# Optimization experiments

Measured on AMD Instinct MI355X. Metric: run time of the kernel, lower is better.

## Reference

```python
import jax, jax.numpy as jnp
import numpy as np

D = 400   # d_model
H = 16    # num heads
KD = 400  # keras MHA key_dim (per-head dim)
GU = 1800 # GRU units
EPS = 1e-6


def _ln(x, g, b):
    m = jnp.mean(x, -1, keepdims=True)
    v = jnp.mean((x - m) ** 2, -1, keepdims=True)
    return (x - m) * jax.lax.rsqrt(v + EPS) * g + b


def _gru_step(x, K, RK, B):
    # Single timestep keras GRU (reset_after=True, activation=elu, h0=0).
    h0 = jnp.zeros((x.shape[0], RK.shape[0]), x.dtype)
    xz, xr, xh = jnp.split(x @ K + B[0], 3, axis=-1)
    rz, rr, rh = jnp.split(h0 @ RK + B[1], 3, axis=-1)
    z = jax.nn.sigmoid(xz + rz)
    r = jax.nn.sigmoid(xr + rr)
    hh = jax.nn.elu(xh + r * rh)
    return z * h0 + (1.0 - z) * hh


def _forward(x, Wq, bq, Wk, bk, Wv, bv, Wo, bo, ln1_g, ln1_b,
             ffn_w1, ffn_b1, ffn_w2, ffn_b2, ln2_g, ln2_b,
             gru_fk, gru_frk, gru_fb, gru_bk, gru_brk, gru_bb,
             d2_w, d2_b, d4_w, d4_b, out_w, out_b):
    # The original python loop over growing prefixes is equivalent to one
    # batched encoder pass over inputs[1:, -1:, :] (seq_len==1, so MHA is
    # per-batch-element independent), with the raw row inputs[0] prepended.
    xe = x[1:, -1:, :]  # [N-1, 1, D]
    q = jnp.einsum('bsd,dhk->bshk', xe, Wq) + bq
    k = jnp.einsum('bsd,dhk->bshk', xe, Wk) + bk
    v = jnp.einsum('bsd,dhk->bshk', xe, Wv) + bv
    logits = jnp.einsum('bqhk,bmhk->bhqm', q, k) / jnp.sqrt(jnp.float32(KD))
    probs = jax.nn.softmax(logits, axis=-1)  # trivially ones (seq=1)
    ctx = jnp.einsum('bhqm,bmhk->bqhk', probs, v)
    attn = jnp.einsum('bqhk,hkd->bqd', ctx, Wo) + bo
    out1 = _ln(xe + attn, ln1_g, ln1_b)
    ffn = jax.nn.relu(out1 @ ffn_w1 + ffn_b1) @ ffn_w2 + ffn_b2
    enc = _ln(out1 + ffn, ln2_g, ln2_b)  # [N-1, 1, D]
    output = jnp.concatenate([x[:1, -1:, :], enc], axis=0)  # [N, 1, D]
    upd = jnp.concatenate([x, output], axis=1)              # [N, 4, D]
    flat = upd.reshape(x.shape[0], -1)                      # [N, 1600]
    # frozen cite_cos_sim_model (inference: dropout layers are identity)
    hf = _gru_step(flat, gru_fk, gru_frk, gru_fb)
    hb = _gru_step(flat, gru_bk, gru_brk, gru_bb)
    x1 = jnp.concatenate([hf, hb], axis=-1)   # [N, 3600]
    x3 = jax.nn.elu(x1 @ d2_w + d2_b)         # [N, 1800]
    x5 = jax.nn.elu(x3 @ d4_w + d4_b)         # [N, 1800]
    cat = jnp.concatenate([x1, x3, x5], axis=-1)  # [N, 7200]
    return cat @ out_w + out_b                # [N, 140]


def setup_inputs() -> dict:
    key = jax.random.key(0)
    shapes = {
        'Wq': (D, H, KD), 'bq': (H, KD), 'Wk': (D, H, KD), 'bk': (H, KD),
        'Wv': (D, H, KD), 'bv': (H, KD), 'Wo': (H, KD, D), 'bo': (D,),
        'ln1_b': (D,), 'ffn_w1': (D, 2), 'ffn_b1': (2,), 'ffn_w2': (2, D),
        'ffn_b2': (D,), 'ln2_b': (D,),
        'gru_fk': (1600, 3 * GU), 'gru_frk': (GU, 3 * GU), 'gru_fb': (2, 3 * GU),
        'gru_bk': (1600, 3 * GU), 'gru_brk': (GU, 3 * GU), 'gru_bb': (2, 3 * GU),
        'd2_w': (2 * GU, GU), 'd2_b': (GU,), 'd4_w': (GU, GU), 'd4_b': (GU,),
        'out_w': (4 * GU, 140), 'out_b': (140,),
    }
    keys = jax.random.split(key, len(shapes) + 1)
    inp = {'x': jax.random.normal(keys[0], (16384, 3, D), jnp.float32)}
    for i, (name, sh) in enumerate(shapes.items()):
        inp[name] = jax.random.normal(keys[i + 1], sh, jnp.float32) * 0.02
    inp['ln1_g'] = jnp.ones((D,), jnp.float32)
    inp['ln2_g'] = jnp.ones((D,), jnp.float32)
    return inp


def reference(x, Wq, bq, Wk, bk, Wv, bv, Wo, bo, ln1_g, ln1_b,
              ffn_w1, ffn_b1, ffn_w2, ffn_b2, ln2_g, ln2_b,
              gru_fk, gru_frk, gru_fb, gru_bk, gru_brk, gru_bb,
              d2_w, d2_b, d4_w, d4_b, out_w, out_b):
    return _forward(x, Wq, bq, Wk, bk, Wv, bv, Wo, bo, ln1_g, ln1_b,
                    ffn_w1, ffn_b1, ffn_w2, ffn_b2, ln2_g, ln2_b,
                    gru_fk, gru_frk, gru_fb, gru_bk, gru_brk, gru_bb,
                    d2_w, d2_b, d4_w, d4_b, out_w, out_b)
```

## Files before the change

kernel.cpp:

```cpp
#include <hip/hip_runtime.h>
#include <hip/hip_bf16.h>

typedef unsigned short u16;
using bf16x8 = __attribute__((ext_vector_type(8))) short;
using f32x4  = __attribute__((ext_vector_type(4))) float;

#define CM 2048
#define NC 8

#define P_LN1G 0
#define P_LN1B 400
#define P_FW1  800
#define P_FB1  1600
#define P_FW2  1602
#define P_FB2  2402
#define P_LN2G 2802
#define P_LN2B 3202
#define P_GFB  3602
#define P_GBB  14402
#define P_BV   25202
#define P_BO   31602
#define P_OB   32002
#define P_END  32142

__device__ __forceinline__ u16 f2bf(float f) {
  unsigned u = __float_as_uint(f);
  unsigned r = u + 0x7FFFu + ((u >> 16) & 1u);
  return (u16)(r >> 16);
}
__device__ __forceinline__ float bf2f(u16 h) {
  return __uint_as_float(((unsigned)h) << 16);
}

__device__ __forceinline__ void gl_lds16(const u16* g, u16* l) {
  __builtin_amdgcn_global_load_lds(
      (__attribute__((address_space(1))) void*)g,
      (__attribute__((address_space(3))) void*)l, 16, 0, 0);
}

__global__ void detect_dtype(int* flag, const void* x) {
  if (threadIdx.x == 0 && blockIdx.x == 0) {
    const u16* p = (const u16*)x;
    int cnt = 0;
    for (int i = 0; i < 64; i++) {
      int e = (p[2 * i] >> 7) & 0xFF;
      if (e >= 0x70 && e <= 0x85) cnt++;
    }
    *flag = (cnt >= 32) ? 1 : 0;
  }
}

__global__ void canon_bf(u16* __restrict__ dst, const void* __restrict__ src,
                         int n, const int* __restrict__ flag) {
  int i = blockIdx.x * 256 + threadIdx.x;
  if (i >= n) return;
  dst[i] = (*flag) ? ((const u16*)src)[i] : f2bf(((const float*)src)[i]);
}

__global__ void canon_x_rows(u16* __restrict__ dst, const void* __restrict__ src,
                             long base, int n, const int* __restrict__ flag) {
  int i = blockIdx.x * 256 + threadIdx.x;
  if (i >= n) return;
  long j = base + i;
  dst[i] = (*flag) ? ((const u16*)src)[j] : f2bf(((const float*)src)[j]);
}

__global__ void canon_f32k(float* __restrict__ dst, const void* __restrict__ src,
                           int n, const int* __restrict__ flag) {
  int i = blockIdx.x * 256 + threadIdx.x;
  if (i >= n) return;
  dst[i] = (*flag) ? bf2f(((const u16*)src)[i]) : ((const float*)src)[i];
}

__global__ void f32_to_bf(u16* __restrict__ dst, const float* __restrict__ src, int n) {
  int i = blockIdx.x * 256 + threadIdx.x;
  if (i < n) dst[i] = f2bf(src[i]);
}

template <int EPI, bool CL>
__global__ __launch_bounds__(256) void gemm_bt(
    const u16* __restrict__ A, const u16* __restrict__ Bt, void* __restrict__ Cv,
    const float* __restrict__ bias, int M, int N, int K, int lda, int ldb, int ldc,
    const u16* aend)
{
  __shared__ u16 lsA[128 * 32];
  __shared__ u16 lsB[128 * 32];
  const int tid = threadIdx.x;
  const int m0 = blockIdx.x * 128, n0 = blockIdx.y * 128;
  const int wave = tid >> 6, lane = tid & 63;
  const int wm = (wave >> 1) << 6, wn = (wave & 1) << 6;
  const int quad = lane >> 4, l16 = lane & 15;

  int ra = m0 + (tid >> 2);       if (ra > M - 1) ra = M - 1;
  int ra2 = m0 + 64 + (tid >> 2); if (ra2 > M - 1) ra2 = M - 1;
  int rb = n0 + (tid >> 2);       if (rb > N - 1) rb = N - 1;
  int rb2 = n0 + 64 + (tid >> 2); if (rb2 > N - 1) rb2 = N - 1;
  const u16* Ag  = A + (size_t)ra * lda + (tid & 3) * 8;
  const u16* Ag2 = A + (size_t)ra2 * lda + (tid & 3) * 8;
  const u16* Bg  = Bt + (size_t)rb * ldb + (tid & 3) * 8;
  const u16* Bg2 = Bt + (size_t)rb2 * ldb + (tid & 3) * 8;
  u16* la = lsA + tid * 8;
  u16* lb = lsB + tid * 8;

  f32x4 acc[4][4];
#pragma unroll
  for (int i = 0; i < 4; i++)
#pragma unroll
    for (int j = 0; j < 4; j++) acc[i][j] = (f32x4){0.f, 0.f, 0.f, 0.f};

  for (int k0 = 0; k0 < K; k0 += 32) {
    __syncthreads();
    const u16* pa  = Ag + k0;
    const u16* pa2 = Ag2 + k0;
    if (CL) { if (pa > aend) pa = aend; if (pa2 > aend) pa2 = aend; }
    gl_lds16(pa, la);
    gl_lds16(pa2, la + 2048);
    gl_lds16(Bg + k0, lb);
    gl_lds16(Bg2 + k0, lb + 2048);
    __syncthreads();
    bf16x8 af[4], bfv[4];
#pragma unroll
    for (int t = 0; t < 4; t++) {
      af[t]  = *(const bf16x8*)(lsA + ((wm + t * 16 + l16) << 5) + (quad << 3));
      bfv[t] = *(const bf16x8*)(lsB + ((wn + t * 16 + l16) << 5) + (quad << 3));
    }
#pragma unroll
    for (int mt = 0; mt < 4; mt++)
#pragma unroll
      for (int nt = 0; nt < 4; nt++)
        acc[mt][nt] = __builtin_amdgcn_mfma_f32_16x16x32_bf16(af[mt], bfv[nt], acc[mt][nt], 0, 0, 0);
  }

#pragma unroll
  for (int mt = 0; mt < 4; mt++)
#pragma unroll
    for (int r = 0; r < 4; r++) {
      const int row = m0 + wm + mt * 16 + quad * 4 + r;
      if (row < M) {
#pragma unroll
        for (int nt = 0; nt < 4; nt++) {
          const int col = n0 + wn + nt * 16 + l16;
          if (col < N) {
            float v = acc[mt][nt][r];
            if (EPI == 0) ((u16*)Cv)[(size_t)row * ldc + col] = f2bf(v);
            if (EPI == 1) ((float*)Cv)[(size_t)row * ldc + col] = v + bias[col];
            if (EPI == 2) {
              float p = v + bias[col];
              ((u16*)Cv)[(size_t)row * ldc + col] = f2bf(p > 0.f ? p : expm1f(p));
            }
          }
        }
      }
    }
}

__global__ __launch_bounds__(256) void gemm_bt_sk(
    const u16* __restrict__ A, const u16* __restrict__ Bt, float* __restrict__ outf,
    int M, int N, int K, int lda, int ldb, int ldc)
{
  __shared__ u16 lsA[128 * 32];
  __shared__ u16 lsB[128 * 32];
  const int tid = threadIdx.x;
  const int m0 = blockIdx.x * 128, n0 = blockIdx.y * 128;
  const int wave = tid >> 6, lane = tid & 63;
  const int wm = (wave >> 1) << 6, wn = (wave & 1) << 6;
  const int quad = lane >> 4, l16 = lane & 15;
  const int S = K >> 5, kz = blockIdx.z, KS = gridDim.z;
  const int s0 = (S * kz) / KS, s1 = (S * (kz + 1)) / KS;

  int ra = m0 + (tid >> 2);       if (ra > M - 1) ra = M - 1;
  int ra2 = m0 + 64 + (tid >> 2); if (ra2 > M - 1) ra2 = M - 1;
  int rb = n0 + (tid >> 2);       if (rb > N - 1) rb = N - 1;
  int rb2 = n0 + 64 + (tid >> 2); if (rb2 > N - 1) rb2 = N - 1;
  const u16* Ag  = A + (size_t)ra * lda + (tid & 3) * 8;
  const u16* Ag2 = A + (size_t)ra2 * lda + (tid & 3) * 8;
  const u16* Bg  = Bt + (size_t)rb * ldb + (tid & 3) * 8;
  const u16* Bg2 = Bt + (size_t)rb2 * ldb + (tid & 3) * 8;
  u16* la = lsA + tid * 8;
  u16* lb = lsB + tid * 8;

  f32x4 acc[4][4];
#pragma unroll
  for (int i = 0; i < 4; i++)
#pragma unroll
    for (int j = 0; j < 4; j++) acc[i][j] = (f32x4){0.f, 0.f, 0.f, 0.f};

  for (int s = s0; s < s1; ++s) {
    const int k0 = s << 5;
    __syncthreads();
    gl_lds16(Ag + k0, la);
    gl_lds16(Ag2 + k0, la + 2048);
    gl_lds16(Bg + k0, lb);
    gl_lds16(Bg2 + k0, lb + 2048);
    __syncthreads();
    bf16x8 af[4], bfv[4];
#pragma unroll
    for (int t = 0; t < 4; t++) {
      af[t]  = *(const bf16x8*)(lsA + ((wm + t * 16 + l16) << 5) + (quad << 3));
      bfv[t] = *(const bf16x8*)(lsB + ((wn + t * 16 + l16) << 5) + (quad << 3));
    }
#pragma unroll
    for (int mt = 0; mt < 4; mt++)
#pragma unroll
      for (int nt = 0; nt < 4; nt++)
        acc[mt][nt] = __builtin_amdgcn_mfma_f32_16x16x32_bf16(af[mt], bfv[nt], acc[mt][nt], 0, 0, 0);
  }

#pragma unroll
  for (int mt = 0; mt < 4; mt++)
#pragma unroll
    for (int r = 0; r < 4; r++) {
      const int row = m0 + wm + mt * 16 + quad * 4 + r;
      if (row < M) {
#pragma unroll
        for (int nt = 0; nt < 4; nt++) {
          const int col = n0 + wn + nt * 16 + l16;
          if (col < N) atomicAdd(&outf[(size_t)row * ldc + col], acc[mt][nt][r]);
        }
      }
    }
}

__global__ __launch_bounds__(256) void transpose_bf(
    u16* __restrict__ dst, const void* __restrict__ src, int SR, int SC, int DR, int DC,
    const int* __restrict__ flag)
{
  __shared__ u16 t[32][33];
  const int fl = *flag;
  const int tx = threadIdx.x & 31, ty = threadIdx.x >> 5;
  const int j0 = blockIdx.x << 5;
  const int i0 = blockIdx.y << 5;
#pragma unroll
  for (int s = 0; s < 32; s += 8) {
    int sr = j0 + ty + s, sc = i0 + tx;
    u16 v = 0;
    if (sr < SR && sc < SC) {
      size_t idx = (size_t)sr * SC + sc;
      v = fl ? ((const u16*)src)[idx] : f2bf(((const float*)src)[idx]);
    }
    t[ty + s][tx] = v;
  }
  __syncthreads();
#pragma unroll
  for (int s = 0; s < 32; s += 8) {
    int dr = i0 + ty + s, dc = j0 + tx;
    if (dr < DR && dc < DC) dst[(size_t)dr * DC + dc] = t[tx][ty + s];
  }
}

__global__ void build_outT(u16* __restrict__ dst, const void* __restrict__ ow,
                           const int* __restrict__ flag) {
  const int fl = *flag;
  int idx = blockIdx.x * 256 + threadIdx.x;
  if (idx >= 140 * 7264) return;
  int o = idx / 7264, c = idx - o * 7264;
  long si = -1;
  if (c < 3600) si = (long)c * 140 + o;
  else if (c >= 3616 && c < 5416) si = (long)(c - 16) * 140 + o;
  else if (c >= 5440 && c < 7240) si = (long)(c - 40) * 140 + o;
  u16 v = 0;
  if (si >= 0) v = fl ? ((const u16*)ow)[si] : f2bf(((const float*)ow)[si]);
  dst[idx] = v;
}

__global__ void zero_u32(unsigned* p, int n) {
  int i = blockIdx.x * 256 + threadIdx.x;
  if (i < n) p[i] = 0;
}

__global__ void zero_catpads(u16* cat, int rows) {
  int idx = blockIdx.x * 256 + threadIdx.x;
  if (idx >= rows * 64) return;
  int b = idx >> 6, t = idx & 63;
  int col = t < 16 ? 3600 + t : (t < 40 ? 5400 + t : 7200 + t);
  cat[(size_t)b * 7264 + col] = 0;
}

__global__ void init_outf(float* __restrict__ outf, const u16* __restrict__ pbuf) {
  int i = blockIdx.x * 256 + threadIdx.x;
  if (i < 16384 * 140) outf[i] = bf2f(pbuf[P_OB + i % 140]);
}

__device__ __forceinline__ void block_sum2(float& a, float& b, float* red, int t) {
#pragma unroll
  for (int o = 32; o > 0; o >>= 1) { a += __shfl_down(a, o, 64); b += __shfl_down(b, o, 64); }
  __syncthreads();
  if ((t & 63) == 0) { red[t >> 6] = a; red[4 + (t >> 6)] = b; }
  __syncthreads();
  a = red[0] + red[1] + red[2] + red[3];
  b = red[4] + red[5] + red[6] + red[7];
}

__global__ __launch_bounds__(256) void c0_kernel(float* c0, const u16* __restrict__ WoT,
                                                 const u16* __restrict__ pbuf) {
  __shared__ float red[8];
  int d = blockIdx.x, t = threadIdx.x;
  const u16* row = WoT + (size_t)d * 6400;
  const u16* bv = pbuf + P_BV;
  float s = 0.f;
  for (int j = t; j < 6400; j += 256) s += bf2f(bv[j]) * bf2f(row[j]);
  float dummy = 0.f;
  block_sum2(s, dummy, red, t);
  if (t == 0) c0[d] = s + bf2f(pbuf[P_BO + d]);
}

__global__ __launch_bounds__(256) void enc_rows(
    const u16* __restrict__ xc, const float* __restrict__ attn,
    const u16* __restrict__ pbuf, u16* __restrict__ flatc, int r0)
{
  __shared__ float red[8];
  const int li = blockIdx.x, t = threadIdx.x;
  const int gr = r0 + li;
  const u16* xr = xc + (size_t)li * 1200;
  u16* fr = flatc + (size_t)li * 1600;
  if (t < 150) ((uint4*)fr)[t] = ((const uint4*)xr)[t];
  if (gr == 0) {
    if (t < 50) ((uint4*)(fr + 1200))[t] = ((const uint4*)(xr + 800))[t];
    return;
  }
  const u16* xe = xr + 800;
  const float* at = attn + (size_t)li * 400;
  const u16 *g1 = pbuf + P_LN1G, *b1 = pbuf + P_LN1B, *fw1 = pbuf + P_FW1,
            *fb1v = pbuf + P_FB1, *fw2 = pbuf + P_FW2, *fb2v = pbuf + P_FB2,
            *g2 = pbuf + P_LN2G, *b2 = pbuf + P_LN2B;
  const int i1 = t + 256;
  float a0 = bf2f(xe[t]) + at[t];
  float a1 = 0.f;
  if (i1 < 400) a1 = bf2f(xe[i1]) + at[i1];
  float s = a0 + a1, ss = a0 * a0 + a1 * a1;
  block_sum2(s, ss, red, t);
  float mean = s * (1.f / 400.f);
  float var = ss * (1.f / 400.f) - mean * mean;
  float rstd = rsqrtf(var + 1e-6f);
  float o0 = (a0 - mean) * rstd * bf2f(g1[t]) + bf2f(b1[t]);
  float o1 = 0.f;
  if (i1 < 400) o1 = (a1 - mean) * rstd * bf2f(g1[i1]) + bf2f(b1[i1]);
  float d0 = o0 * bf2f(fw1[2 * t]), d1 = o0 * bf2f(fw1[2 * t + 1]);
  if (i1 < 400) { d0 += o1 * bf2f(fw1[2 * i1]); d1 += o1 * bf2f(fw1[2 * i1 + 1]); }
  block_sum2(d0, d1, red, t);
  float t0 = d0 + bf2f(fb1v[0]); t0 = t0 > 0.f ? t0 : 0.f;
  float t1 = d1 + bf2f(fb1v[1]); t1 = t1 > 0.f ? t1 : 0.f;
  float c0v = o0 + t0 * bf2f(fw2[t]) + t1 * bf2f(fw2[400 + t]) + bf2f(fb2v[t]);
  float c1v = 0.f;
  if (i1 < 400) c1v = o1 + t0 * bf2f(fw2[i1]) + t1 * bf2f(fw2[400 + i1]) + bf2f(fb2v[i1]);
  s = c0v + c1v; ss = c0v * c0v + c1v * c1v;
  block_sum2(s, ss, red, t);
  mean = s * (1.f / 400.f);
  var = ss * (1.f / 400.f) - mean * mean;
  rstd = rsqrtf(var + 1e-6f);
  u16* dr = fr + 1200;
  dr[t] = f2bf((c0v - mean) * rstd * bf2f(g2[t]) + bf2f(b2[t]));
  if (i1 < 400) dr[i1] = f2bf((c1v - mean) * rstd * bf2f(g2[i1]) + bf2f(b2[i1]));
}

__global__ __launch_bounds__(256) void gru_act(
    const u16* __restrict__ G, int ldg, const u16* __restrict__ pbuf, int boff,
    u16* __restrict__ cat, int off, int rows)
{
  int idx = blockIdx.x * 256 + threadIdx.x;
  if (idx >= rows * 1800) return;
  int b = idx / 1800, u = idx - b * 1800;
  const u16* g = G + (size_t)b * ldg;
  const u16* B = pbuf + boff;
  float xz = bf2f(g[u]) + bf2f(B[u]) + bf2f(B[5400 + u]);
  float xr = bf2f(g[1800 + u]) + bf2f(B[1800 + u]) + bf2f(B[7200 + u]);
  float xh = bf2f(g[3600 + u]) + bf2f(B[3600 + u]);
  float rh = bf2f(B[9000 + u]);
  float z = 1.f / (1.f + expf(-xz));
  float r = 1.f / (1.f + expf(-xr));
  float pre = xh + r * rh;
  float hh = pre > 0.f ? pre : expm1f(pre);
  cat[(size_t)b * 7264 + off + u] = f2bf((1.f - z) * hh);
}

extern "C" void kernel_launch(void* const* d_in, const int* in_sizes, int n_in,
                              void* d_out, int out_size, void* d_ws, size_t ws_size,
                              hipStream_t stream) {
  static const int MAP_DICT[22] = {5,6,7,8, 9,10,11,12,13,14, 15,17,18,20, 21,22,23,24, 25,26, 27,28};
  static const int MAP_SIG[22]  = {5,6,7,8, 10,11,12,13,14,16, 17,19,20,22, 23,24,25,26, 27,28, 9,15};
  const int* MAP = (in_sizes[15] > 100000) ? MAP_DICT : MAP_SIG;

  const void* x    = d_in[0];
  const void* Wv   = d_in[MAP[0]];
  const void* bv   = d_in[MAP[1]];
  const void* Wo   = d_in[MAP[2]];
  const void* bo   = d_in[MAP[3]];
  const void* ln1b = d_in[MAP[4]];
  const void* fw1  = d_in[MAP[5]];
  const void* fb1  = d_in[MAP[6]];
  const void* fw2  = d_in[MAP[7]];
  const void* fb2  = d_in[MAP[8]];
  const void* ln2b = d_in[MAP[9]];
  const void* gfk  = d_in[MAP[10]];
  const void* gfb  = d_in[MAP[11]];
  const void* gbk  = d_in[MAP[12]];
  const void* gbb  = d_in[MAP[13]];
  const void* d2w  = d_in[MAP[14]];
  const void* d2b  = d_in[MAP[15]];
  const void* d4w  = d_in[MAP[16]];
  const void* d4b  = d_in[MAP[17]];
  const void* ow   = d_in[MAP[18]];
  const void* ob   = d_in[MAP[19]];
  const void* ln1g = d_in[MAP[20]];
  const void* ln2g = d_in[MAP[21]];
  float* outf = (float*)d_out;

  unsigned char* base = (unsigned char*)d_ws;
  size_t off = 0;
  auto take = [&](size_t bytes) -> void* {
    void* p = base + off;
    off += (bytes + 255) & ~(size_t)255;
    return p;
  };
  u16*   KfT   = (u16*)take((size_t)5400 * 1600 * 2);
  u16*   KbT   = (u16*)take((size_t)5400 * 1600 * 2);
  u16*   d2T   = (u16*)take((size_t)1800 * 3616 * 2);
  u16*   d4T   = (u16*)take((size_t)1800 * 1824 * 2);
  u16*   outT  = (u16*)take((size_t)140 * 7264 * 2);
  u16*   WoT   = (u16*)take((size_t)400 * 6400 * 2);
  u16*   MT    = (u16*)take((size_t)400 * 416 * 2);
  float* MTf   = (float*)take((size_t)400 * 416 * 4);
  u16*   pbuf  = (u16*)take((size_t)P_END * 2);
  int*   flag  = (int*)take(256);
  float* c0    = (float*)take(400 * 4);
  float* d2bf  = (float*)take(1800 * 4);
  float* d4bf  = (float*)take(1800 * 4);

  int CMV = 0;
  {
    const size_t avail  = ws_size > off ? ws_size - off : 0;
    const size_t perrow = (size_t)(1600 + 10800 + 7264) * 2;
    const size_t margin = (size_t)4 << 20;
    if      (avail >= (size_t)16384 * perrow + margin) CMV = 16384;
    else if (avail >= (size_t)8192  * perrow + margin) CMV = 8192;
    else if (avail >= (size_t)4096  * perrow + margin) CMV = 4096;
    else if (avail >= (size_t)2048  * perrow + margin) CMV = 2048;
  }

  u16 *flatc, *Gc, *catc;
  if (CMV) {
    flatc = (u16*)take((size_t)CMV * 1600 * 2);
    Gc    = (u16*)take((size_t)CMV * 10800 * 2);
    catc  = (u16*)take((size_t)CMV * 7264 * 2);
  } else {
    flatc = (u16*)take((size_t)CM * 1600 * 2);
    Gc    = (u16*)take((size_t)CM * 5400 * 2);
    catc  = (u16*)take((size_t)CM * 7264 * 2);
  }
  const int rows = CMV ? CMV : CM;
  float* attnc = (float*)Gc;
  u16*   xc    = (u16*)((unsigned char*)Gc + (size_t)rows * 1600);
  u16*   Wvc   = catc;

  detect_dtype<<<1, 64, 0, stream>>>(flag, x);
  canon_bf<<<2, 256, 0, stream>>>(pbuf + P_LN1G, ln1g, 400, flag);
  canon_bf<<<2, 256, 0, stream>>>(pbuf + P_LN1B, ln1b, 400, flag);
  canon_bf<<<4, 256, 0, stream>>>(pbuf + P_FW1, fw1, 800, flag);
  canon_bf<<<1, 256, 0, stream>>>(pbuf + P_FB1, fb1, 2, flag);
  canon_bf<<<4, 256, 0, stream>>>(pbuf + P_FW2, fw2, 800, flag);
  canon_bf<<<2, 256, 0, stream>>>(pbuf + P_FB2, fb2, 400, flag);
  canon_bf<<<2, 256, 0, stream>>>(pbuf + P_LN2G, ln2g, 400, flag);
  canon_bf<<<2, 256, 0, stream>>>(pbuf + P_LN2B, ln2b, 400, flag);
  canon_bf<<<43, 256, 0, stream>>>(pbuf + P_GFB, gfb, 10800, flag);
  canon_bf<<<43, 256, 0, stream>>>(pbuf + P_GBB, gbb, 10800, flag);
  canon_bf<<<25, 256, 0, stream>>>(pbuf + P_BV, bv, 6400, flag);
  canon_bf<<<2, 256, 0, stream>>>(pbuf + P_BO, bo, 400, flag);
  canon_bf<<<1, 256, 0, stream>>>(pbuf + P_OB, ob, 140, flag);
  canon_f32k<<<8, 256, 0, stream>>>(d2bf, d2b, 1800, flag);
  canon_f32k<<<8, 256, 0, stream>>>(d4bf, d4b, 1800, flag);

  transpose_bf<<<dim3(50, 169), 256, 0, stream>>>(KfT, gfk, 1600, 5400, 5400, 1600, flag);
  transpose_bf<<<dim3(50, 169), 256, 0, stream>>>(KbT, gbk, 1600, 5400, 5400, 1600, flag);
  transpose_bf<<<dim3(113, 57), 256, 0, stream>>>(d2T, d2w, 3600, 1800, 1800, 3616, flag);
  transpose_bf<<<dim3(57, 57), 256, 0, stream>>>(d4T, d4w, 1800, 1800, 1800, 1824, flag);
  transpose_bf<<<dim3(200, 13), 256, 0, stream>>>(WoT, Wo, 6400, 400, 400, 6400, flag);
  build_outT<<<(140 * 7264 + 255) / 256, 256, 0, stream>>>(outT, ow, flag);
  init_outf<<<(16384 * 140 + 255) / 256, 256, 0, stream>>>(outf, pbuf);
  c0_kernel<<<400, 256, 0, stream>>>(c0, WoT, pbuf);

  canon_bf<<<10000, 256, 0, stream>>>(Wvc, Wv, 2560000, flag);
  zero_u32<<<(166400 + 255) / 256, 256, 0, stream>>>((unsigned*)MTf, 166400);
  gemm_bt_sk<<<dim3(4, 4, 16), 256, 0, stream>>>(WoT, Wvc, MTf,
      400, 400, 6400, 6400, 6400, 416);
  f32_to_bf<<<(166400 + 255) / 256, 256, 0, stream>>>(MT, MTf, 166400);

  if (CMV) {
    zero_catpads<<<(CMV * 64 + 255) / 256, 256, 0, stream>>>(catc, CMV);
    const int nchunk = 16384 / CMV;
    for (int c = 0; c < nchunk; ++c) {
      const long r0 = (long)c * CMV;
      canon_x_rows<<<(CMV * 1200 + 255) / 256, 256, 0, stream>>>(
          xc, x, r0 * 1200, CMV * 1200, flag);
      gemm_bt<1, true><<<dim3(CMV / 128, 4), 256, 0, stream>>>(
          xc + 800, MT, attnc, c0, CMV, 400, 416, 1200, 416, 400,
          xc + (size_t)CMV * 1200 - 8);
      enc_rows<<<CMV, 256, 0, stream>>>(xc, attnc, pbuf, flatc, (int)r0);
      gemm_bt<0, false><<<dim3(CMV / 128, 85), 256, 0, stream>>>(
          flatc, KfT, Gc, nullptr, CMV, 10800, 1600, 1600, 1600, 10800, nullptr);
      gru_act<<<(CMV * 1800 + 255) / 256, 256, 0, stream>>>(
          Gc, 10800, pbuf, P_GFB, catc, 0, CMV);
      gru_act<<<(CMV * 1800 + 255) / 256, 256, 0, stream>>>(
          Gc + 5400, 10800, pbuf, P_GBB, catc, 1800, CMV);
      gemm_bt<2, false><<<dim3(CMV / 128, 15), 256, 0, stream>>>(
          catc, d2T, catc + 3616, d2bf, CMV, 1800, 3616, 7264, 3616, 7264, nullptr);
      gemm_bt<2, false><<<dim3(CMV / 128, 15), 256, 0, stream>>>(
          catc + 3616, d4T, catc + 5440, d4bf, CMV, 1800, 1824, 7264, 1824, 7264, nullptr);
      gemm_bt_sk<<<dim3(CMV / 128, 2, 8), 256, 0, stream>>>(
          catc, outT, outf + (size_t)r0 * 140, CMV, 140, 7264, 7264, 7264, 140);
    }
  } else {
    zero_catpads<<<(CM * 64 + 255) / 256, 256, 0, stream>>>(catc, CM);
    for (int c = 0; c < NC; ++c) {
      const int r0 = c * CM;
      canon_x_rows<<<(CM * 1200 + 255) / 256, 256, 0, stream>>>(
          xc, x, (long)r0 * 1200, CM * 1200, flag);
      gemm_bt<1, true><<<dim3(CM / 128, 4), 256, 0, stream>>>(
          xc + 800, MT, attnc, c0, CM, 400, 416, 1200, 416, 400,
          xc + (size_t)CM * 1200 - 8);
      enc_rows<<<CM, 256, 0, stream>>>(xc, attnc, pbuf, flatc, r0);
      gemm_bt<0, false><<<dim3(CM / 128, 43), 256, 0, stream>>>(
          flatc, KfT, Gc, nullptr, CM, 5400, 1600, 1600, 1600, 5400, nullptr);
      gru_act<<<(CM * 1800 + 255) / 256, 256, 0, stream>>>(
          Gc, 5400, pbuf, P_GFB, catc, 0, CM);
      gemm_bt<0, false><<<dim3(CM / 128, 43), 256, 0, stream>>>(
          flatc, KbT, Gc, nullptr, CM, 5400, 1600, 1600, 1600, 5400, nullptr);
      gru_act<<<(CM * 1800 + 255) / 256, 256, 0, stream>>>(
          Gc, 5400, pbuf, P_GBB, catc, 1800, CM);
      gemm_bt<2, false><<<dim3(CM / 128, 15), 256, 0, stream>>>(
          catc, d2T, catc + 3616, d2bf, CM, 1800, 3616, 7264, 3616, 7264, nullptr);
      gemm_bt<2, false><<<dim3(CM / 128, 15), 256, 0, stream>>>(
          catc + 3616, d4T, catc + 5440, d4bf, CM, 1800, 1824, 7264, 1824, 7264, nullptr);
      gemm_bt_sk<<<dim3(CM / 128, 2, 8), 256, 0, stream>>>(
          catc, outT, outf + (size_t)r0 * 140, CM, 140, 7264, 7264, 7264, 140);
    }
  }
}
```

Measured before the change: 2.445 ms.

## Add 256x256-tile double-buffered GEMM kernel for GRU input projection

New measurement: 2.282 ms. -6.7%, faster.

```diff
diff --git a/kernel.cpp b/kernel.cpp
--- a/kernel.cpp
+++ b/kernel.cpp
@@ -144,6 +144,103 @@
             float v = acc[mt][nt][r];
             if (EPI == 0) ((u16*)Cv)[(size_t)row * ldc + col] = f2bf(v);
             if (EPI == 1) ((float*)Cv)[(size_t)row * ldc + col] = v + bias[col];
+            if (EPI == 2) {
+              float p = v + bias[col];
+              ((u16*)Cv)[(size_t)row * ldc + col] = f2bf(p > 0.f ? p : expm1f(p));
+            }
+          }
+        }
+      }
+    }
+}
+
+template <int EPI>
+__global__ __launch_bounds__(512, 2) void gemm256_bt(
+    const u16* __restrict__ A, const u16* __restrict__ Bt, void* __restrict__ Cv,
+    const float* __restrict__ bias, int M, int N, int K, int lda, int ldb, int ldc)
+{
+  __shared__ u16 lds8[65536];
+  const int tid = threadIdx.x;
+  const int m0 = blockIdx.x * 256, n0 = blockIdx.y * 256;
+  const int wave = tid >> 6, lane = tid & 63;
+  const int wm = (wave >> 2) * 128;
+  const int wn = (wave & 3) * 64;
+  const int quad = lane >> 4, l16 = lane & 15;
+
+  const int srow = tid >> 3;
+  const int sblk = ((tid & 7) ^ (srow & 7)) * 8;
+  const u16* Ag[4];
+  const u16* Bg[4];
+#pragma unroll
+  for (int i = 0; i < 4; i++) {
+    int raw = m0 + i * 64 + srow; if (raw > M - 1) raw = M - 1;
+    int rbw = n0 + i * 64 + srow; if (rbw > N - 1) rbw = N - 1;
+    Ag[i] = A  + (size_t)raw * lda + sblk;
+    Bg[i] = Bt + (size_t)rbw * ldb + sblk;
+  }
+
+  f32x4 acc[8][4];
+#pragma unroll
+  for (int i = 0; i < 8; i++)
+#pragma unroll
+    for (int j = 0; j < 4; j++) acc[i][j] = (f32x4){0.f, 0.f, 0.f, 0.f};
+
+  const int nT = K >> 6;
+#pragma unroll
+  for (int i = 0; i < 4; i++) gl_lds16(Ag[i], lds8 + i * 4096 + tid * 8);
+#pragma unroll
+  for (int i = 0; i < 4; i++) gl_lds16(Bg[i], lds8 + 16384 + i * 4096 + tid * 8);
+
+  int c = 0;
+  for (int t = 0; t < nT; ++t) {
+    __builtin_amdgcn_s_barrier();
+    if (t + 1 < nT) {
+      const int k1 = (t + 1) << 6;
+      u16* dst = lds8 + (c ^ 1) * 32768;
+#pragma unroll
+      for (int i = 0; i < 4; i++) gl_lds16(Ag[i] + k1, dst + i * 4096 + tid * 8);
+#pragma unroll
+      for (int i = 0; i < 4; i++) gl_lds16(Bg[i] + k1, dst + 16384 + i * 4096 + tid * 8);
+      asm volatile("s_waitcnt vmcnt(8)" ::: "memory");
+    } else {
+      asm volatile("s_waitcnt vmcnt(0)" ::: "memory");
+    }
+    __builtin_amdgcn_s_barrier();
+    const u16* lA = lds8 + c * 32768;
+    const u16* lB = lA + 16384;
+#pragma unroll
+    for (int kk = 0; kk < 2; kk++) {
+      const int ch = kk * 4 + quad;
+      bf16x8 af[8], bv[4];
+#pragma unroll
+      for (int mt = 0; mt < 8; mt++)
+        af[mt] = *(const bf16x8*)(lA + (wm + mt * 16 + l16) * 64 + ((ch ^ (l16 & 7)) * 8));
+#pragma unroll
+      for (int nt = 0; nt < 4; nt++)
+        bv[nt] = *(const bf16x8*)(lB + (wn + nt * 16 + l16) * 64 + ((ch ^ (l16 & 7)) * 8));
+      __builtin_amdgcn_s_setprio(1);
+#pragma unroll
+      for (int mt = 0; mt < 8; mt++)
+#pragma unroll
+        for (int nt = 0; nt < 4; nt++)
+          acc[mt][nt] = __builtin_amdgcn_mfma_f32_16x16x32_bf16(af[mt], bv[nt], acc[mt][nt], 0, 0, 0);
+      __builtin_amdgcn_s_setprio(0);
+    }
+    c ^= 1;
+  }
+
+#pragma unroll
+  for (int mt = 0; mt < 8; mt++)
+#pragma unroll
+    for (int r = 0; r < 4; r++) {
+      const int row = m0 + wm + mt * 16 + quad * 4 + r;
+      if (row < M) {
+#pragma unroll
+        for (int nt = 0; nt < 4; nt++) {
+          const int col = n0 + wn + nt * 16 + l16;
+          if (col < N) {
+            float v = acc[mt][nt][r];
+            if (EPI == 0) ((u16*)Cv)[(size_t)row * ldc + col] = f2bf(v);
             if (EPI == 2) {
               float p = v + bias[col];
               ((u16*)Cv)[(size_t)row * ldc + col] = f2bf(p > 0.f ? p : expm1f(p));
@@ -495,8 +592,8 @@
           xc + 800, MT, attnc, c0, CMV, 400, 416, 1200, 416, 400,
           xc + (size_t)CMV * 1200 - 8);
       enc_rows<<<CMV, 256, 0, stream>>>(xc, attnc, pbuf, flatc, (int)r0);
-      gemm_bt<0, false><<<dim3(CMV / 128, 85), 256, 0, stream>>>(
-          flatc, KfT, Gc, nullptr, CMV, 10800, 1600, 1600, 1600, 10800, nullptr);
+      gemm256_bt<0><<<dim3(CMV / 256, 43), 512, 0, stream>>>(
+          flatc, KfT, Gc, nullptr, CMV, 10800, 1600, 1600, 1600, 10800);
       gru_act<<<(CMV * 1800 + 255) / 256, 256, 0, stream>>>(
           Gc, 10800, pbuf, P_GFB, catc, 0, CMV);
       gru_act<<<(CMV * 1800 + 255) / 256, 256, 0, stream>>>(
```
